# Performance work log

Hardware: AMD Instinct MI355X
Metric: run time of the kernel (lower is better)

## Reference

```python
import jax, jax.numpy as jnp
import numpy as np

N, E, NMASK, NC = 50000, 600000, 10000, 16
DIMS = [128, 96, 64]
EPS = 1e-5


def _sage(x, src, dst, ew, deg_pos, Wp, bp, Ws, Wn, b):
    # DGL SAGEConv 'pool': m_e = relu(fc_pool(h_src)) * w_e ; neigh = max_e->v m_e
    p = jax.nn.relu(x @ Wp.T + bp)              # [N, din]
    m = p[src] * ew[:, None]                    # [E, din]
    neigh = jax.ops.segment_max(m, dst, num_segments=N)
    neigh = jnp.where(deg_pos, neigh, 0.0)      # zero in-degree -> 0 (DGL convention)
    return jax.nn.relu(x @ Ws.T + neigh @ Wn.T + b)


def setup_inputs() -> dict:
    key = jax.random.key(0)
    ks = iter(jax.random.split(key, 64))
    inp = {}
    inp["x"] = jax.random.normal(next(ks), (N, DIMS[0]), jnp.float32)
    inp["src"] = jax.random.randint(next(ks), (E,), 0, N)
    inp["dst"] = jax.random.randint(next(ks), (E,), 0, N)
    inp["ew"] = jax.random.uniform(next(ks), (E,), jnp.float32)
    inp["mask_nodes"] = jax.random.permutation(next(ks), N)[:NMASK]
    inp["mask_token"] = jax.random.normal(next(ks), (1, DIMS[0]), jnp.float32) * 0.02

    def lin(k, o, i):
        return jax.random.normal(k, (o, i), jnp.float32) * (1.0 / np.sqrt(i))

    enc_pairs = list(zip(DIMS[:-1], DIMS[1:]))              # (128,96),(96,64)
    dec_pairs = [(o, i) for (i, o) in reversed(enc_pairs)]  # (64,96),(96,128)
    for name, pairs in (("enc", enc_pairs), ("dec", dec_pairs)):
        for l, (di, do) in enumerate(pairs):
            inp[f"{name}{l}_Wp"] = lin(next(ks), di, di)
            inp[f"{name}{l}_bp"] = jnp.zeros((di,), jnp.float32)
            inp[f"{name}{l}_Ws"] = lin(next(ks), do, di)
            inp[f"{name}{l}_Wn"] = lin(next(ks), do, di)
            inp[f"{name}{l}_b"] = jnp.zeros((do,), jnp.float32)
    H = DIMS[-1]
    inp["W_e2d"] = lin(next(ks), H, H)
    inp["Wnp"] = lin(next(ks), NC, H)
    inp["bnp"] = jnp.zeros((NC,), jnp.float32)
    inp["ln_g"] = jnp.ones((NC,), jnp.float32)
    inp["ln_b"] = jnp.zeros((NC,), jnp.float32)
    return inp


def reference(x, src, dst, ew, mask_nodes, mask_token,
              enc0_Wp, enc0_bp, enc0_Ws, enc0_Wn, enc0_b,
              enc1_Wp, enc1_bp, enc1_Ws, enc1_Wn, enc1_b,
              dec0_Wp, dec0_bp, dec0_Ws, dec0_Wn, dec0_b,
              dec1_Wp, dec1_bp, dec1_Ws, dec1_Wn, dec1_b,
              W_e2d, Wnp, bnp, ln_g, ln_b):
    deg = jax.ops.segment_sum(jnp.ones((E,), jnp.float32), dst, num_segments=N)
    deg_pos = (deg > 0)[:, None]
    # mask: out_x[mask]=0 then += enc_mask_token  ==  set to token row
    h = x.at[mask_nodes].set(mask_token[0])
    h = _sage(h, src, dst, ew, deg_pos, enc0_Wp, enc0_bp, enc0_Ws, enc0_Wn, enc0_b)
    h = _sage(h, src, dst, ew, deg_pos, enc1_Wp, enc1_bp, enc1_Ws, enc1_Wn, enc1_b)
    # dropout(p=0) is identity
    z = h @ Wnp.T + bnp                              # node_pred linear
    mu = jnp.mean(z, -1, keepdims=True)
    var = jnp.var(z, -1, keepdims=True)
    n_scores = (z - mu) * jax.lax.rsqrt(var + EPS) * ln_g + ln_b
    r = h @ W_e2d.T                                  # encoder_to_decoder (no bias)
    r = _sage(r, src, dst, ew, deg_pos, dec0_Wp, dec0_bp, dec0_Ws, dec0_Wn, dec0_b)
    r = _sage(r, src, dst, ew, deg_pos, dec1_Wp, dec1_bp, dec1_Ws, dec1_Wn, dec1_b)
    return (r[mask_nodes], x[mask_nodes], n_scores)
```

## Files before the change

### kernel.cpp

```cpp
#include <hip/hip_runtime.h>

#define EPS_LN 1e-5f

typedef __attribute__((ext_vector_type(4))) float f32x4;
typedef __attribute__((ext_vector_type(4))) int i32x4;

__device__ inline unsigned short f2bf_rne(float x) {
  unsigned int u = __float_as_uint(x);
  unsigned int r = u + 0x7fffu + ((u >> 16) & 1u);
  return (unsigned short)(r >> 16);
}

__device__ inline float4 bf4_to_f4(uint2 u) {
  float4 f;
  f.x = __uint_as_float(u.x << 16);
  f.y = __uint_as_float(u.x & 0xffff0000u);
  f.z = __uint_as_float(u.y << 16);
  f.w = __uint_as_float(u.y & 0xffff0000u);
  return f;
}

__device__ inline uint2 f4_to_bf4(float4 v) {
  uint2 o;
  o.x = (unsigned)f2bf_rne(v.x) | ((unsigned)f2bf_rne(v.y) << 16);
  o.y = (unsigned)f2bf_rne(v.z) | ((unsigned)f2bf_rne(v.w) << 16);
  return o;
}

__global__ __launch_bounds__(256) void copy_bf16_kernel(const float4* __restrict__ in,
                                                        uint2* __restrict__ out, int n4) {
  int i = blockIdx.x * 256 + threadIdx.x;
  if (i < n4) out[i] = f4_to_bf4(in[i]);
}

__global__ __launch_bounds__(256) void mask_scatter_kernel(const int* __restrict__ mn,
                                                           const float* __restrict__ token,
                                                           unsigned short* __restrict__ H,
                                                           int nmask) {
  int gid = blockIdx.x * 256 + threadIdx.x;
  if (gid >= nmask * 32) return;
  int i = gid >> 5;
  int c4 = (gid & 31) << 2;
  int r = mn[i];
  float4 t = *(const float4*)(token + c4);
  *(uint2*)(H + (size_t)r * 128 + c4) = f4_to_bf4(t);
}

__global__ __launch_bounds__(256) void hist_kernel(const int* __restrict__ dst,
                                                   int* __restrict__ deg, int nE) {
  int e = blockIdx.x * 256 + threadIdx.x;
  if (e < nE) atomicAdd(deg + dst[e], 1);
}

#define SCAN_CHUNK 1024

__global__ __launch_bounds__(256) void blocksum_kernel(const int* __restrict__ deg,
                                                       int* __restrict__ bsum, int n) {
  __shared__ int red[256];
  int base = blockIdx.x * SCAN_CHUNK;
  int tid = threadIdx.x;
  int s = 0;
#pragma unroll
  for (int t = 0; t < SCAN_CHUNK / 256; ++t) {
    int g = base + tid + t * 256;
    if (g < n) s += deg[g];
  }
  red[tid] = s;
  __syncthreads();
  for (int ofs = 128; ofs > 0; ofs >>= 1) {
    if (tid < ofs) red[tid] += red[tid + ofs];
    __syncthreads();
  }
  if (tid == 0) bsum[blockIdx.x] = red[0];
}

__global__ __launch_bounds__(64) void bscan_kernel(const int* __restrict__ bsum,
                                                   int* __restrict__ bbase,
                                                   int* __restrict__ off_n, int nb) {
  int tid = threadIdx.x;
  int v = (tid < nb) ? bsum[tid] : 0;
  int incl = v;
#pragma unroll
  for (int ofs = 1; ofs < 64; ofs <<= 1) {
    int u = __shfl_up(incl, ofs, 64);
    if (tid >= ofs) incl += u;
  }
  if (tid < nb) bbase[tid] = incl - v;
  if (tid == nb - 1) off_n[0] = incl;
}

__global__ __launch_bounds__(256) void chunkscan_kernel(const int* __restrict__ deg,
                                                        const int* __restrict__ bbase,
                                                        int* __restrict__ off, int n) {
  __shared__ int part[256];
  int tid = threadIdx.x;
  int base = blockIdx.x * SCAN_CHUNK;
  int g0 = base + tid * 4;
  int loc[4];
  int s = 0;
#pragma unroll
  for (int j = 0; j < 4; ++j) {
    int g = g0 + j;
    int d = (g < n) ? deg[g] : 0;
    loc[j] = s;
    s += d;
  }
  part[tid] = s;
  __syncthreads();
  for (int ofs = 1; ofs < 256; ofs <<= 1) {
    int v = 0;
    if (tid >= ofs) v = part[tid - ofs];
    __syncthreads();
    if (tid >= ofs) part[tid] += v;
    __syncthreads();
  }
  int pre = (tid == 0) ? 0 : part[tid - 1];
  int b = bbase[blockIdx.x] + pre;
#pragma unroll
  for (int j = 0; j < 4; ++j) {
    int g = g0 + j;
    if (g < n) off[g] = b + loc[j];
  }
}

__global__ __launch_bounds__(256) void scatter_kernel(const int* __restrict__ src,
                                                      const int* __restrict__ dst,
                                                      const float* __restrict__ ew,
                                                      const int* __restrict__ off,
                                                      int* __restrict__ cur,
                                                      int2* __restrict__ esw, int nE) {
  int e = blockIdx.x * 256 + threadIdx.x;
  if (e >= nE) return;
  int d = dst[e];
  int pos = off[d] + atomicAdd(cur + d, 1);
  esw[pos] = make_int2(src[e], __float_as_int(ew[e]));
}

__global__ __launch_bounds__(256) void neigh_csr_kernel(
    const unsigned short* __restrict__ P, const int* __restrict__ off,
    const int2* __restrict__ esw,
    unsigned short* __restrict__ neigh, int din, int lanes, int nN) {
  int gid = blockIdx.x * 256 + threadIdx.x;
  int v = gid / lanes;
  int c = (gid - v * lanes) << 2;
  if (v >= nN) return;
  int jlo = off[v], jhi = off[v + 1];
  float4 m0 = make_float4(0.f, 0.f, 0.f, 0.f);
  float4 m1 = m0, m2 = m0, m3 = m0;
  int j = jlo;
  for (; j + 4 <= jhi; j += 4) {
    int2 e0 = esw[j], e1 = esw[j + 1], e2 = esw[j + 2], e3 = esw[j + 3];
    uint2 q0 = *(const uint2*)(P + (size_t)e0.x * din + c);
    uint2 q1 = *(const uint2*)(P + (size_t)e1.x * din + c);
    uint2 q2 = *(const uint2*)(P + (size_t)e2.x * din + c);
    uint2 q3 = *(const uint2*)(P + (size_t)e3.x * din + c);
    float w0 = __int_as_float(e0.y), w1 = __int_as_float(e1.y);
    float w2 = __int_as_float(e2.y), w3 = __int_as_float(e3.y);
    float4 p0 = bf4_to_f4(q0), p1 = bf4_to_f4(q1);
    float4 p2 = bf4_to_f4(q2), p3 = bf4_to_f4(q3);
    m0.x = fmaxf(m0.x, p0.x * w0); m0.y = fmaxf(m0.y, p0.y * w0);
    m0.z = fmaxf(m0.z, p0.z * w0); m0.w = fmaxf(m0.w, p0.w * w0);
    m1.x = fmaxf(m1.x, p1.x * w1); m1.y = fmaxf(m1.y, p1.y * w1);
    m1.z = fmaxf(m1.z, p1.z * w1); m1.w = fmaxf(m1.w, p1.w * w1);
    m2.x = fmaxf(m2.x, p2.x * w2); m2.y = fmaxf(m2.y, p2.y * w2);
    m2.z = fmaxf(m2.z, p2.z * w2); m2.w = fmaxf(m2.w, p2.w * w2);
    m3.x = fmaxf(m3.x, p3.x * w3); m3.y = fmaxf(m3.y, p3.y * w3);
    m3.z = fmaxf(m3.z, p3.z * w3); m3.w = fmaxf(m3.w, p3.w * w3);
  }
  for (; j < jhi; ++j) {
    int2 e = esw[j];
    float w = __int_as_float(e.y);
    float4 p = bf4_to_f4(*(const uint2*)(P + (size_t)e.x * din + c));
    m0.x = fmaxf(m0.x, p.x * w); m0.y = fmaxf(m0.y, p.y * w);
    m0.z = fmaxf(m0.z, p.z * w); m0.w = fmaxf(m0.w, p.w * w);
  }
  m0.x = fmaxf(fmaxf(m0.x, m1.x), fmaxf(m2.x, m3.x));
  m0.y = fmaxf(fmaxf(m0.y, m1.y), fmaxf(m2.y, m3.y));
  m0.z = fmaxf(fmaxf(m0.z, m1.z), fmaxf(m2.z, m3.z));
  m0.w = fmaxf(fmaxf(m0.w, m1.w), fmaxf(m2.w, m3.w));
  float4 mm = make_float4(m0.x, m0.y, m0.z, m0.w);
  *(uint2*)(neigh + (size_t)v * din + c) = f4_to_bf4(mm);
}

__global__ __launch_bounds__(256) void matmul_small_kernel(const float* __restrict__ A,
                                                           const float* __restrict__ B,
                                                           float* __restrict__ C,
                                                           int M, int K, int N) {
  int idx = blockIdx.x * 256 + threadIdx.x;
  if (idx >= M * N) return;
  int o = idx / N, i = idx - o * N;
  float s = 0.f;
  for (int k = 0; k < K; ++k) s += A[o * K + k] * B[k * N + i];
  C[idx] = s;
}

__device__ inline void mfma_b16(f32x4& acc, i32x4 a, i32x4 b) {
  asm volatile("v_mfma_f32_16x16x32_bf16 %0, %1, %2, %0"
               : "+v"(acc)
               : "v"(a), "v"(b));
}

__device__ inline void split_bf16(float x, unsigned short& hi, unsigned short& lo) {
  unsigned int bits = __float_as_uint(x);
  hi = (unsigned short)(bits >> 16);
  float hif = __uint_as_float((unsigned int)hi << 16);
  float res = x - hif;
  lo = (unsigned short)(__float_as_uint(res) >> 16);
}

struct SplitWArgs {
  const float* src[12];
  unsigned short* dh[12];
  unsigned short* dl[12];
  int n[12];
};

__global__ __launch_bounds__(256) void split_w_kernel(SplitWArgs a) {
  int m = blockIdx.y;
  int i = (blockIdx.x * 256 + threadIdx.x) * 4;
  if (i >= a.n[m]) return;
  float4 v = *(const float4*)(a.src[m] + i);
  unsigned short h[4], l[4];
  split_bf16(v.x, h[0], l[0]);
  split_bf16(v.y, h[1], l[1]);
  split_bf16(v.z, h[2], l[2]);
  split_bf16(v.w, h[3], l[3]);
  *(uint2*)(a.dh[m] + i) = make_uint2((unsigned)h[0] | ((unsigned)h[1] << 16),
                                      (unsigned)h[2] | ((unsigned)h[3] << 16));
  *(uint2*)(a.dl[m] + i) = make_uint2((unsigned)l[0] | ((unsigned)l[1] << 16),
                                      (unsigned)l[2] | ((unsigned)l[3] << 16));
}

template <int TNT>
__global__ __launch_bounds__(256) void mfma_gemm_kernel(
    const unsigned short* __restrict__ A1, const unsigned short* __restrict__ Wh1,
    const unsigned short* __restrict__ Wl1, int k1,
    const unsigned short* __restrict__ A2, const unsigned short* __restrict__ Wh2,
    const unsigned short* __restrict__ Wl2, int k2,
    const float* __restrict__ bias, int relu,
    unsigned short* __restrict__ C, int nrows) {
  constexpr int BN = TNT * 16;
  constexpr int WS = 136;
  __shared__ __align__(16) unsigned short Wh[BN][WS];
  __shared__ __align__(16) unsigned short Wl[BN][WS];

  const int tid = threadIdx.x;
  const int lane = tid & 63;
  const int wv = tid >> 6;
  const int lr = lane & 15;
  const int lg = lane >> 4;
  const int row0 = blockIdx.x * 64;
  const int gra = row0 + wv * 16 + lr;

  f32x4 acc[TNT];
#pragma unroll
  for (int t = 0; t < TNT; ++t) acc[t] = (f32x4)(0.f);

  for (int pass = 0; pass < 2; ++pass) {
    const unsigned short* A = pass ? A2 : A1;
    if (A == nullptr) continue;
    const unsigned short* Whp = pass ? Wh2 : Wh1;
    const unsigned short* Wlp = pass ? Wl2 : Wl1;
    const int K = pass ? k2 : k1;

    if (pass) __syncthreads();
    {
      int tot8 = BN * K / 8;
      for (int i = tid; i < tot8; i += 256) {
        int e0 = i * 8;
        int col = e0 / K;
        int kk = e0 - col * K;
        *(uint4*)&Wh[col][kk] = *(const uint4*)(Whp + e0);
        *(uint4*)&Wl[col][kk] = *(const uint4*)(Wlp + e0);
      }
    }
    __syncthreads();

    for (int cb = 0; cb < K; cb += 32) {
      i32x4 a_h = (i32x4)(0);
      if (gra < nrows) a_h = *(const i32x4*)(A + (size_t)gra * K + cb + lg * 8);
#pragma unroll
      for (int t = 0; t < TNT; ++t) {
        i32x4 b_h = *(const i32x4*)&Wh[t * 16 + lr][cb + lg * 8];
        i32x4 b_l = *(const i32x4*)&Wl[t * 16 + lr][cb + lg * 8];
        mfma_b16(acc[t], a_h, b_h);
        mfma_b16(acc[t], a_h, b_l);
      }
    }
  }

  asm volatile("s_nop 7\n\ts_nop 7" ::);

#pragma unroll
  for (int t = 0; t < TNT; ++t) {
    int c = t * 16 + lr;
    float bv = bias ? bias[c] : 0.f;
#pragma unroll
    for (int q = 0; q < 4; ++q) {
      int r = row0 + wv * 16 + lg * 4 + q;
      if (r < nrows) {
        float v = acc[t][q] + bv;
        if (relu) v = fmaxf(v, 0.f);
        C[(size_t)r * BN + c] = f2bf_rne(v);
      }
    }
  }
}

__global__ __launch_bounds__(256) void nodepred_ln_kernel(
    const unsigned short* __restrict__ H, const float* __restrict__ Wnp,
    const float* __restrict__ bnp, const float* __restrict__ g,
    const float* __restrict__ lb, float* __restrict__ out, int nrows) {
  __shared__ float hs[16][64];
  int tid = threadIdx.x;
  int row0 = blockIdx.x * 16;
  {
    int r = tid >> 4;
    int c4 = (tid & 15) << 2;
    int gr = row0 + r;
    float4 v = make_float4(0.f, 0.f, 0.f, 0.f);
    if (gr < nrows) v = bf4_to_f4(*(const uint2*)(H + (size_t)gr * 64 + c4));
    *(float4*)&hs[r][c4] = v;
  }
  __syncthreads();
  int r = tid >> 4, j = tid & 15;
  float z = bnp[j];
  const float* wrow = Wnp + j * 64;
#pragma unroll 8
  for (int k = 0; k < 64; ++k) z += hs[r][k] * wrow[k];
  float s = z, s2 = z * z;
#pragma unroll
  for (int m = 1; m < 16; m <<= 1) {
    s += __shfl_xor(s, m, 16);
    s2 += __shfl_xor(s2, m, 16);
  }
  float mu = s * (1.f / 16.f);
  float var = s2 * (1.f / 16.f) - mu * mu;
  float o = (z - mu) * rsqrtf(var + EPS_LN) * g[j] + lb[j];
  int gr = row0 + r;
  if (gr < nrows) out[(size_t)gr * 16 + j] = o;
}

__global__ __launch_bounds__(256) void gather_out_kernel(
    const int* __restrict__ mn, const unsigned short* __restrict__ R,
    const float* __restrict__ X,
    float* __restrict__ o1, float* __restrict__ o2, int nmask) {
  int gid = blockIdx.x * 256 + threadIdx.x;
  if (gid >= nmask * 32) return;
  int i = gid >> 5, c4 = (gid & 31) << 2;
  int r = mn[i];
  float4 rv = bf4_to_f4(*(const uint2*)(R + (size_t)r * 128 + c4));
  *(float4*)(o1 + (size_t)i * 128 + c4) = rv;
  *(float4*)(o2 + (size_t)i * 128 + c4) = *(const float4*)(X + (size_t)r * 128 + c4);
}

static void launch_gemm(const unsigned short* A1, const unsigned short* Wh1,
                        const unsigned short* Wl1, int k1,
                        const unsigned short* A2, const unsigned short* Wh2,
                        const unsigned short* Wl2, int k2,
                        const float* bias, int relu,
                        unsigned short* C, int m, int nrows, hipStream_t s) {
  int blocks = (nrows + 63) / 64;
  switch (m) {
    case 128:
      mfma_gemm_kernel<8><<<blocks, 256, 0, s>>>(A1, Wh1, Wl1, k1, A2, Wh2, Wl2, k2,
                                                 bias, relu, C, nrows);
      break;
    case 96:
      mfma_gemm_kernel<6><<<blocks, 256, 0, s>>>(A1, Wh1, Wl1, k1, A2, Wh2, Wl2, k2,
                                                 bias, relu, C, nrows);
      break;
    case 64:
      mfma_gemm_kernel<4><<<blocks, 256, 0, s>>>(A1, Wh1, Wl1, k1, A2, Wh2, Wl2, k2,
                                                 bias, relu, C, nrows);
      break;
  }
}

extern "C" void kernel_launch(void* const* d_in, const int* in_sizes, int n_in,
                              void* d_out, int out_size, void* d_ws, size_t ws_size,
                              hipStream_t stream) {
  const float* x = (const float*)d_in[0];
  const int* src = (const int*)d_in[1];
  const int* dst = (const int*)d_in[2];
  const float* ew = (const float*)d_in[3];
  const int* mn = (const int*)d_in[4];
  const float* token = (const float*)d_in[5];

  const float* W[20];
  for (int i = 0; i < 20; ++i) W[i] = (const float*)d_in[6 + i];
  const float* W_e2d = (const float*)d_in[26];
  const float* Wnp = (const float*)d_in[27];
  const float* bnp = (const float*)d_in[28];
  const float* ln_g = (const float*)d_in[29];
  const float* ln_b = (const float*)d_in[30];

  const int Nn = in_sizes[0] / 128;
  const int E = in_sizes[1];
  const int nmask = in_sizes[4];
  const int nb = (Nn + SCAN_CHUNK - 1) / SCAN_CHUNK;

  unsigned short* bufA = (unsigned short*)d_ws;
  unsigned short* bufB = bufA + (size_t)Nn * 128;
  unsigned short* pool16 = bufB + (size_t)Nn * 128;
  unsigned short* neigh16 = pool16 + (size_t)Nn * 128;
  int* deg = (int*)(neigh16 + (size_t)Nn * 128);
  int* cur = deg + Nn;
  int2* esw = (int2*)(cur + Nn);
  int* off = (int*)(esw + E);
  int* bsum = off + Nn + 1;
  int* bbase = bsum + 64;
  float* WpP = (float*)(bbase + 64);
  float* WsP = WpP + 64 * 64;
  unsigned short* wplanes =
      (unsigned short*)(((uintptr_t)(WsP + 96 * 64) + 15) & ~(uintptr_t)15);

  matmul_small_kernel<<<(64 * 64 + 255) / 256, 256, 0, stream>>>(W[10], W_e2d, WpP, 64, 64, 64);
  matmul_small_kernel<<<(96 * 64 + 255) / 256, 256, 0, stream>>>(W[12], W_e2d, WsP, 96, 64, 64);

  const int msz[12] = {128 * 128, 96 * 128, 96 * 128, 96 * 96, 64 * 96, 64 * 96,
                       64 * 64,  96 * 64,  96 * 64,  96 * 96, 128 * 96, 128 * 96};
  const float* msrc[12] = {W[0], W[2], W[3], W[5], W[7], W[8],
                           WpP,  WsP,  W[13], W[15], W[17], W[18]};
  int mtot = 0;
  int moff[12];
  for (int i = 0; i < 12; ++i) { moff[i] = mtot; mtot += msz[i]; }
  unsigned short* wh_[12];
  unsigned short* wl_[12];
  SplitWArgs sa;
  for (int i = 0; i < 12; ++i) {
    wh_[i] = wplanes + moff[i];
    wl_[i] = wplanes + mtot + moff[i];
    sa.src[i] = msrc[i];
    sa.dh[i] = wh_[i];
    sa.dl[i] = wl_[i];
    sa.n[i] = msz[i];
  }
  {
    dim3 grid((128 * 128 / 4 + 255) / 256, 12);
    split_w_kernel<<<grid, 256, 0, stream>>>(sa);
  }

  hipMemsetAsync(deg, 0, (size_t)Nn * 2 * sizeof(int), stream);
  hist_kernel<<<(E + 255) / 256, 256, 0, stream>>>(dst, deg, E);
  blocksum_kernel<<<nb, 256, 0, stream>>>(deg, bsum, Nn);
  bscan_kernel<<<1, 64, 0, stream>>>(bsum, bbase, off + Nn, nb);
  chunkscan_kernel<<<nb, 256, 0, stream>>>(deg, bbase, off, Nn);
  scatter_kernel<<<(E + 255) / 256, 256, 0, stream>>>(src, dst, ew, off, cur, esw, E);

  {
    int n4 = Nn * 128 / 4;
    copy_bf16_kernel<<<(n4 + 255) / 256, 256, 0, stream>>>((const float4*)x, (uint2*)bufA, n4);
    mask_scatter_kernel<<<(nmask * 32 + 255) / 256, 256, 0, stream>>>(mn, token, bufA, nmask);
  }

  auto run_sage = [&](int ip, int is, int in_, const float* bp, const float* b,
                      int din, int dout) {
    launch_gemm(bufA, wh_[ip], wl_[ip], din, nullptr, nullptr, nullptr, 0,
                bp, 1, pool16, din, Nn, stream);
    int lanes = din >> 2;
    long long tot = (long long)Nn * lanes;
    int nblocks = (int)((tot + 255) / 256);
    neigh_csr_kernel<<<nblocks, 256, 0, stream>>>(pool16, off, esw, neigh16, din, lanes, Nn);
    launch_gemm(bufA, wh_[is], wl_[is], din, neigh16, wh_[in_], wl_[in_], din,
                b, 1, bufB, dout, Nn, stream);
    unsigned short* t = bufA; bufA = bufB; bufB = t;
  };

  run_sage(0, 1, 2, W[1], W[4], 128, 96);
  run_sage(3, 4, 5, W[6], W[9], 96, 64);

  float* out_r = (float*)d_out;
  float* out_x = out_r + (size_t)nmask * 128;
  float* out_ns = out_x + (size_t)nmask * 128;
  nodepred_ln_kernel<<<(Nn + 15) / 16, 256, 0, stream>>>(bufA, Wnp, bnp, ln_g, ln_b, out_ns, Nn);

  run_sage(6, 7, 8, W[11], W[14], 64, 96);
  run_sage(9, 10, 11, W[16], W[19], 96, 128);

  gather_out_kernel<<<(nmask * 32 + 255) / 256, 256, 0, stream>>>(mn, bufA, x, out_r, out_x, nmask);
}
```

Measured before the change: 378.1 us.

## Two-pass bucketed CSR scatter and 8-wide bf16 gathers in neighbor max

The edge scatter into CSR now runs in two passes. Edges are first bucketed by dst>>7 into a staging array, then a second pass places them at their final per-node slots. Because staged edges are grouped by bucket, the second pass writes and updates its atomics with better locality than direct random per-node placement. The neighbor-max kernel also now gives each thread 8 bf16 channels with 16-byte loads instead of 4 with 8-byte loads, halving thread count and increasing bytes per gather; in exchange it adds an extra pass and staging buffer over all edges and more registers per thread.

Measured after the change: 565.3 us. 1.5x slower.

```diff
diff --git a/kernel.cpp b/kernel.cpp
--- a/kernel.cpp
+++ b/kernel.cpp
@@ -123,17 +123,27 @@
   }
 }
 
-__global__ __launch_bounds__(256) void scatter_kernel(const int* __restrict__ src,
-                                                      const int* __restrict__ dst,
-                                                      const float* __restrict__ ew,
-                                                      const int* __restrict__ off,
-                                                      int* __restrict__ cur,
-                                                      int2* __restrict__ esw, int nE) {
+__global__ __launch_bounds__(256) void bucket_scatter_kernel(
+    const int* __restrict__ src, const int* __restrict__ dst,
+    const float* __restrict__ ew, const int* __restrict__ off,
+    int* __restrict__ bcur, int4* __restrict__ stage, int nE) {
   int e = blockIdx.x * 256 + threadIdx.x;
   if (e >= nE) return;
   int d = dst[e];
-  int pos = off[d] + atomicAdd(cur + d, 1);
-  esw[pos] = make_int2(src[e], __float_as_int(ew[e]));
+  int b = d >> 7;
+  int base = off[b << 7];
+  int pos = base + atomicAdd(bcur + b, 1);
+  stage[pos] = make_int4(src[e], __float_as_int(ew[e]), d, 0);
+}
+
+__global__ __launch_bounds__(256) void final_scatter_kernel(
+    const int4* __restrict__ stage, const int* __restrict__ off,
+    int* __restrict__ cur, int2* __restrict__ esw, int nE) {
+  int e = blockIdx.x * 256 + threadIdx.x;
+  if (e >= nE) return;
+  int4 s = stage[e];
+  int pos = off[s.z] + atomicAdd(cur + s.z, 1);
+  esw[pos] = make_int2(s.x, s.y);
 }
 
 __global__ __launch_bounds__(256) void neigh_csr_kernel(
@@ -142,44 +152,60 @@
     unsigned short* __restrict__ neigh, int din, int lanes, int nN) {
   int gid = blockIdx.x * 256 + threadIdx.x;
   int v = gid / lanes;
-  int c = (gid - v * lanes) << 2;
+  int c = (gid - v * lanes) << 3;
   if (v >= nN) return;
   int jlo = off[v], jhi = off[v + 1];
-  float4 m0 = make_float4(0.f, 0.f, 0.f, 0.f);
-  float4 m1 = m0, m2 = m0, m3 = m0;
+  float m[8];
+#pragma unroll
+  for (int t = 0; t < 8; ++t) m[t] = 0.f;
+  float n1[8], n2[8], n3[8];
+#pragma unroll
+  for (int t = 0; t < 8; ++t) { n1[t] = 0.f; n2[t] = 0.f; n3[t] = 0.f; }
   int j = jlo;
   for (; j + 4 <= jhi; j += 4) {
     int2 e0 = esw[j], e1 = esw[j + 1], e2 = esw[j + 2], e3 = esw[j + 3];
-    uint2 q0 = *(const uint2*)(P + (size_t)e0.x * din + c);
-    uint2 q1 = *(const uint2*)(P + (size_t)e1.x * din + c);
-    uint2 q2 = *(const uint2*)(P + (size_t)e2.x * din + c);
-    uint2 q3 = *(const uint2*)(P + (size_t)e3.x * din + c);
+    uint4 q0 = *(const uint4*)(P + (size_t)e0.x * din + c);
+    uint4 q1 = *(const uint4*)(P + (size_t)e1.x * din + c);
+    uint4 q2 = *(const uint4*)(P + (size_t)e2.x * din + c);
+    uint4 q3 = *(const uint4*)(P + (size_t)e3.x * din + c);
     float w0 = __int_as_float(e0.y), w1 = __int_as_float(e1.y);
     float w2 = __int_as_float(e2.y), w3 = __int_as_float(e3.y);
-    float4 p0 = bf4_to_f4(q0), p1 = bf4_to_f4(q1);
-    float4 p2 = bf4_to_f4(q2), p3 = bf4_to_f4(q3);
-    m0.x = fmaxf(m0.x, p0.x * w0); m0.y = fmaxf(m0.y, p0.y * w0);
-    m0.z = fmaxf(m0.z, p0.z * w0); m0.w = fmaxf(m0.w, p0.w * w0);
-    m1.x = fmaxf(m1.x, p1.x * w1); m1.y = fmaxf(m1.y, p1.y * w1);
-    m1.z = fmaxf(m1.z, p1.z * w1); m1.w = fmaxf(m1.w, p1.w * w1);
-    m2.x = fmaxf(m2.x, p2.x * w2); m2.y = fmaxf(m2.y, p2.y * w2);
-    m2.z = fmaxf(m2.z, p2.z * w2); m2.w = fmaxf(m2.w, p2.w * w2);
-    m3.x = fmaxf(m3.x, p3.x * w3); m3.y = fmaxf(m3.y, p3.y * w3);
-    m3.z = fmaxf(m3.z, p3.z * w3); m3.w = fmaxf(m3.w, p3.w * w3);
+    float4 a0 = bf4_to_f4(make_uint2(q0.x, q0.y)), b0 = bf4_to_f4(make_uint2(q0.z, q0.w));
+    float4 a1 = bf4_to_f4(make_uint2(q1.x, q1.y)), b1 = bf4_to_f4(make_uint2(q1.z, q1.w));
+    float4 a2 = bf4_to_f4(make_uint2(q2.x, q2.y)), b2 = bf4_to_f4(make_uint2(q2.z, q2.w));
+    float4 a3 = bf4_to_f4(make_uint2(q3.x, q3.y)), b3 = bf4_to_f4(make_uint2(q3.z, q3.w));
+    m[0] = fmaxf(m[0], a0.x * w0); m[1] = fmaxf(m[1], a0.y * w0);
+    m[2] = fmaxf(m[2], a0.z * w0); m[3] = fmaxf(m[3], a0.w * w0);
+    m[4] = fmaxf(m[4], b0.x * w0); m[5] = fmaxf(m[5], b0.y * w0);
+    m[6] = fmaxf(m[6], b0.z * w0); m[7] = fmaxf(m[7], b0.w * w0);
+    n1[0] = fmaxf(n1[0], a1.x * w1); n1[1] = fmaxf(n1[1], a1.y * w1);
+    n1[2] = fmaxf(n1[2], a1.z * w1); n1[3] = fmaxf(n1[3], a1.w * w1);
+    n1[4] = fmaxf(n1[4], b1.x * w1); n1[5] = fmaxf(n1[5], b1.y * w1);
+    n1[6] = fmaxf(n1[6], b1.z * w1); n1[7] = fmaxf(n1[7], b1.w * w1);
+    n2[0] = fmaxf(n2[0], a2.x * w2); n2[1] = fmaxf(n2[1], a2.y * w2);
+    n2[2] = fmaxf(n2[2], a2.z * w2); n2[3] = fmaxf(n2[3], a2.w * w2);
+    n2[4] = fmaxf(n2[4], b2.x * w2); n2[5] = fmaxf(n2[5], b2.y * w2);
+    n2[6] = fmaxf(n2[6], b2.z * w2); n2[7] = fmaxf(n2[7], b2.w * w2);
+    n3[0] = fmaxf(n3[0], a3.x * w3); n3[1] = fmaxf(n3[1], a3.y * w3);
+    n3[2] = fmaxf(n3[2], a3.z * w3); n3[3] = fmaxf(n3[3], a3.w * w3);
+    n3[4] = fmaxf(n3[4], b3.x * w3); n3[5] = fmaxf(n3[5], b3.y * w3);
+    n3[6] = fmaxf(n3[6], b3.z * w3); n3[7] = fmaxf(n3[7], b3.w * w3);
   }
   for (; j < jhi; ++j) {
     int2 e = esw[j];
     float w = __int_as_float(e.y);
-    float4 p = bf4_to_f4(*(const uint2*)(P + (size_t)e.x * din + c));
-    m0.x = fmaxf(m0.x, p.x * w); m0.y = fmaxf(m0.y, p.y * w);
-    m0.z = fmaxf(m0.z, p.z * w); m0.w = fmaxf(m0.w, p.w * w);
-  }
-  m0.x = fmaxf(fmaxf(m0.x, m1.x), fmaxf(m2.x, m3.x));
-  m0.y = fmaxf(fmaxf(m0.y, m1.y), fmaxf(m2.y, m3.y));
-  m0.z = fmaxf(fmaxf(m0.z, m1.z), fmaxf(m2.z, m3.z));
-  m0.w = fmaxf(fmaxf(m0.w, m1.w), fmaxf(m2.w, m3.w));
-  float4 mm = make_float4(m0.x, m0.y, m0.z, m0.w);
-  *(uint2*)(neigh + (size_t)v * din + c) = f4_to_bf4(mm);
+    uint4 q = *(const uint4*)(P + (size_t)e.x * din + c);
+    float4 a = bf4_to_f4(make_uint2(q.x, q.y)), b = bf4_to_f4(make_uint2(q.z, q.w));
+    m[0] = fmaxf(m[0], a.x * w); m[1] = fmaxf(m[1], a.y * w);
+    m[2] = fmaxf(m[2], a.z * w); m[3] = fmaxf(m[3], a.w * w);
+    m[4] = fmaxf(m[4], b.x * w); m[5] = fmaxf(m[5], b.y * w);
+    m[6] = fmaxf(m[6], b.z * w); m[7] = fmaxf(m[7], b.w * w);
+  }
+#pragma unroll
+  for (int t = 0; t < 8; ++t) m[t] = fmaxf(fmaxf(m[t], n1[t]), fmaxf(n2[t], n3[t]));
+  uint2 o0 = f4_to_bf4(make_float4(m[0], m[1], m[2], m[3]));
+  uint2 o1 = f4_to_bf4(make_float4(m[4], m[5], m[6], m[7]));
+  *(uint4*)(neigh + (size_t)v * din + c) = make_uint4(o0.x, o0.y, o1.x, o1.y);
 }
 
 __global__ __launch_bounds__(256) void matmul_small_kernel(const float* __restrict__ A,
@@ -406,11 +432,13 @@
   unsigned short* neigh16 = pool16 + (size_t)Nn * 128;
   int* deg = (int*)(neigh16 + (size_t)Nn * 128);
   int* cur = deg + Nn;
-  int2* esw = (int2*)(cur + Nn);
+  int* bcur = cur + Nn;
+  int2* esw = (int2*)(bcur + 512);
   int* off = (int*)(esw + E);
   int* bsum = off + Nn + 1;
   int* bbase = bsum + 64;
-  float* WpP = (float*)(bbase + 64);
+  int4* stage = (int4*)(((uintptr_t)(bbase + 64) + 15) & ~(uintptr_t)15);
+  float* WpP = (float*)(stage + E);
   float* WsP = WpP + 64 * 64;
   unsigned short* wplanes =
       (unsigned short*)(((uintptr_t)(WsP + 96 * 64) + 15) & ~(uintptr_t)15);
@@ -441,12 +469,13 @@
     split_w_kernel<<<grid, 256, 0, stream>>>(sa);
   }
 
-  hipMemsetAsync(deg, 0, (size_t)Nn * 2 * sizeof(int), stream);
+  hipMemsetAsync(deg, 0, ((size_t)Nn * 2 + 512) * sizeof(int), stream);
   hist_kernel<<<(E + 255) / 256, 256, 0, stream>>>(dst, deg, E);
   blocksum_kernel<<<nb, 256, 0, stream>>>(deg, bsum, Nn);
   bscan_kernel<<<1, 64, 0, stream>>>(bsum, bbase, off + Nn, nb);
   chunkscan_kernel<<<nb, 256, 0, stream>>>(deg, bbase, off, Nn);
-  scatter_kernel<<<(E + 255) / 256, 256, 0, stream>>>(src, dst, ew, off, cur, esw, E);
+  bucket_scatter_kernel<<<(E + 255) / 256, 256, 0, stream>>>(src, dst, ew, off, bcur, stage, E);
+  final_scatter_kernel<<<(E + 255) / 256, 256, 0, stream>>>(stage, off, cur, esw, E);
 
   {
     int n4 = Nn * 128 / 4;
@@ -458,7 +487,7 @@
                       int din, int dout) {
     launch_gemm(bufA, wh_[ip], wl_[ip], din, nullptr, nullptr, nullptr, 0,
                 bp, 1, pool16, din, Nn, stream);
-    int lanes = din >> 2;
+    int lanes = din >> 3;
     long long tot = (long long)Nn * lanes;
     int nblocks = (int)((tot + 255) / 256);
     neigh_csr_kernel<<<nblocks, 256, 0, stream>>>(pool16, off, esw, neigh16, din, lanes, Nn);
```
